# Optimization experiments

Measured on AMD Instinct MI355X. Metric: run time of the kernel, lower is better.

Reference implementation:

```python
import jax, jax.numpy as jnp
import numpy as np

N = 12000       # nodes (Hi-C bins, max_num_nodes)
F_IN = 16       # number_genomic_annotations
HID = 4 * F_IN  # conv1 out = 64
NCLUST = 100    # n_clust
E = 384000      # edges (avg degree 32)


def setup_inputs() -> dict:
    key = jax.random.key(0)
    ks = jax.random.split(key, 8)
    x = jax.random.normal(ks[0], (N, F_IN), dtype=jnp.float32)
    edge_index = jax.random.randint(ks[1], (2, E), 0, N)
    edge_attr = jax.random.uniform(ks[2], (E,), dtype=jnp.float32)
    s1 = 1.0 / np.sqrt(F_IN)
    W1_rel = jax.random.uniform(ks[3], (HID, F_IN), minval=-s1, maxval=s1, dtype=jnp.float32)
    W1_root = jax.random.uniform(ks[4], (HID, F_IN), minval=-s1, maxval=s1, dtype=jnp.float32)
    b1 = jnp.zeros((HID,), jnp.float32)
    s2 = 1.0 / np.sqrt(HID)
    W2_rel = jax.random.uniform(ks[5], (NCLUST, HID), minval=-s2, maxval=s2, dtype=jnp.float32)
    W2_root = jax.random.uniform(ks[6], (NCLUST, HID), minval=-s2, maxval=s2, dtype=jnp.float32)
    b2 = jnp.zeros((NCLUST,), jnp.float32)
    return dict(x=x, edge_index=edge_index, edge_attr=edge_attr,
                W1_rel=W1_rel, W1_root=W1_root, b1=b1,
                W2_rel=W2_rel, W2_root=W2_root, b2=b2)


def _graph_conv(x, src, dst, ew, W_rel, W_root, b):
    # PyG GraphConv (aggr='add'): out = lin_rel(sum_j e_ji * x_j) + lin_root(x)
    msg = x[src] * ew[:, None]                       # [E, F]
    aggr = jax.ops.segment_sum(msg, dst, num_segments=N)  # [N, F]
    return aggr @ W_rel.T + b + x @ W_root.T


def reference(x, edge_index, edge_attr, W1_rel, W1_root, b1, W2_rel, W2_root, b2):
    src, dst = edge_index[0], edge_index[1]
    h = _graph_conv(x, src, dst, edge_attr, W1_rel, W1_root, b1)
    h = jax.nn.relu(h)  # dropout is identity in eval mode
    s_out = _graph_conv(h, src, dst, edge_attr, W2_rel, W2_root, b2)  # [N, NCLUST]

    # to_dense_adj (duplicate edges summed)
    adj = jnp.zeros((N, N), x.dtype).at[src, dst].add(edge_attr)  # [N, N]

    # dense_mincut_pool with S = x (as in the original forward), k = F_IN
    s_mc = jax.nn.softmax(x, axis=-1)      # [N, F_IN]
    as_ = adj @ s_mc                        # [N, F_IN]
    out_adj = s_mc.T @ as_                  # [F_IN, F_IN]
    mincut_num = jnp.trace(out_adj)
    d_flat = adj.sum(-1)                    # [N] degree
    mincut_den = jnp.einsum('ik,i,ik->', s_mc, d_flat, s_mc)  # trace(S^T D S)
    mc = -(mincut_num / mincut_den)

    ss = s_mc.T @ s_mc                      # [F_IN, F_IN]
    i_k = jnp.eye(F_IN, dtype=ss.dtype)
    o = jnp.linalg.norm(ss / jnp.linalg.norm(ss) - i_k / jnp.linalg.norm(i_k))

    return jax.nn.softmax(s_out, axis=-1), mc, o
```

## Files before the change

### kernel.cpp

```cpp
#include <hip/hip_runtime.h>
#include <math.h>

#define N_NODES 12000
#define F_INN 16
#define HIDD 64
#define NCLUST 100
#define NEDGE 384000
#define NBLK_N 47
#define CAP 96
#define EPT 4
#define NTHR_E (NEDGE / EPT)
#define NBLK_E (NTHR_E / 256)
#define NBLK_F1 (N_NODES / 4)

#define OFF_COUNT   0
#define OFF_SCAL    12000
#define ZERO_ELEMS  12002
#define OFF_SSPART  12004
#define OFF_NORM2   24036
#define OFF_W2TREL  36036
#define OFF_W2TROOT 42436
#define OFF_SMC     48836
#define OFF_H       240836
#define OFF_SRCW    1008836

__global__ void zero_kernel(int* __restrict__ ws) {
    int i = blockIdx.x * 256 + threadIdx.x;
    if (i < ZERO_ELEMS) ws[i] = 0;
}

__global__ void phase0_kernel(const float* __restrict__ x, const int* __restrict__ ei,
                              const float* __restrict__ ew, float* __restrict__ smc,
                              float* __restrict__ norm2, int* __restrict__ count,
                              int2* __restrict__ srcw, const float* __restrict__ W2_rel,
                              const float* __restrict__ W2_root, float* __restrict__ w2t_rel,
                              float* __restrict__ w2t_root) {
    __shared__ float fl[6400];
    int t = threadIdx.x;
    int b = blockIdx.x;
    if (b < NBLK_N) {
        int i = b * 256 + t;
        if (i >= N_NODES) return;
        const float4* xr = (const float4*)(x + i * 16);
        float4 r0 = xr[0], r1 = xr[1], r2 = xr[2], r3 = xr[3];
        float v[16] = {r0.x, r0.y, r0.z, r0.w, r1.x, r1.y, r1.z, r1.w,
                       r2.x, r2.y, r2.z, r2.w, r3.x, r3.y, r3.z, r3.w};
        float m = v[0];
#pragma unroll
        for (int k = 1; k < 16; ++k) m = fmaxf(m, v[k]);
        float s = 0.f;
#pragma unroll
        for (int k = 0; k < 16; ++k) { v[k] = __expf(v[k] - m); s += v[k]; }
        float inv = 1.f / s;
        float n2 = 0.f;
#pragma unroll
        for (int k = 0; k < 16; ++k) { v[k] *= inv; n2 += v[k] * v[k]; }
        float4* so = (float4*)(smc + i * 16);
        so[0] = make_float4(v[0], v[1], v[2], v[3]);
        so[1] = make_float4(v[4], v[5], v[6], v[7]);
        so[2] = make_float4(v[8], v[9], v[10], v[11]);
        so[3] = make_float4(v[12], v[13], v[14], v[15]);
        norm2[i] = n2;
    } else if (b < NBLK_N + NBLK_E) {
        int tid = (b - NBLK_N) * 256 + t;
        int e0 = tid * EPT;
        int4 sv = *(const int4*)(ei + e0);
        int4 dv = *(const int4*)(ei + NEDGE + e0);
        float4 wv = *(const float4*)(ew + e0);
        int s[EPT] = {sv.x, sv.y, sv.z, sv.w};
        int d[EPT] = {dv.x, dv.y, dv.z, dv.w};
        float w[EPT] = {wv.x, wv.y, wv.z, wv.w};
        int pos[EPT];
#pragma unroll
        for (int i = 0; i < EPT; ++i) pos[i] = atomicAdd(&count[d[i]], 1);
#pragma unroll
        for (int i = 0; i < EPT; ++i)
            srcw[d[i] * CAP + pos[i]] = make_int2(s[i], __float_as_int(w[i]));
    } else {
        const float* src = (b == NBLK_N + NBLK_E) ? W2_rel : W2_root;
        float* dst = (b == NBLK_N + NBLK_E) ? w2t_rel : w2t_root;
        for (int i = t; i < 6400; i += 256) fl[i] = src[i];
        __syncthreads();
        for (int j = t; j < 6400; j += 256) {
            int kk = j / 100, cl = j - kk * 100;
            dst[j] = fl[cl * 64 + kk];
        }
    }
}

__global__ void fused1_pass2_kernel(const float* __restrict__ x, const int2* __restrict__ srcw,
                                    const int* __restrict__ count, const float* __restrict__ W1_rel,
                                    const float* __restrict__ W1_root, const float* __restrict__ b1,
                                    float* __restrict__ h, const float* __restrict__ smc,
                                    float* __restrict__ sspart, const int* __restrict__ ei,
                                    const float* __restrict__ ew, const float* __restrict__ norm2,
                                    float* __restrict__ scal) {
    __shared__ float shm[4352];
    int t = threadIdx.x;
    int b = blockIdx.x;
    if (b < NBLK_F1) {
        float* wrelT  = shm;
        float* wrootT = shm + 1024;
        float* b1s    = shm + 2048;
        float* aggr   = shm + 2112;
        float* xs     = shm + 2176;
        for (int idx = t; idx < 1024; idx += 256) {
            int f = idx >> 4, k = idx & 15;
            wrelT[(k << 6) + f]  = W1_rel[idx];
            wrootT[(k << 6) + f] = W1_root[idx];
        }
        if (t < 64) b1s[t] = b1[t];
        int w = t >> 6, lane = t & 63;
        int n = b * 4 + w;
        int j = lane >> 4, c = lane & 15;
        int len = count[n];
        const int2* bucket = srcw + n * CAP;
        float acc = 0.f;
        int k = j;
        for (; k + 12 < len; k += 16) {
            int2 p0 = bucket[k], p1 = bucket[k + 4], p2 = bucket[k + 8], p3 = bucket[k + 12];
            float v0 = x[p0.x * 16 + c], v1 = x[p1.x * 16 + c];
            float v2 = x[p2.x * 16 + c], v3 = x[p3.x * 16 + c];
            acc = fmaf(v0, __int_as_float(p0.y), acc);
            acc = fmaf(v1, __int_as_float(p1.y), acc);
            acc = fmaf(v2, __int_as_float(p2.y), acc);
            acc = fmaf(v3, __int_as_float(p3.y), acc);
        }
        for (; k < len; k += 4) {
            int2 p = bucket[k];
            acc = fmaf(x[p.x * 16 + c], __int_as_float(p.y), acc);
        }
        acc += __shfl_down(acc, 32);
        acc += __shfl_down(acc, 16);
        if (lane < 16) { aggr[w * 16 + lane] = acc; xs[w * 16 + lane] = x[n * 16 + lane]; }
        __syncthreads();
        float o = b1s[lane];
#pragma unroll
        for (int kk = 0; kk < 16; ++kk)
            o = fmaf(aggr[w * 16 + kk], wrelT[(kk << 6) + lane],
                     fmaf(xs[w * 16 + kk], wrootT[(kk << 6) + lane], o));
        h[n * 64 + lane] = fmaxf(o, 0.f);
    } else if (b < NBLK_F1 + NBLK_N) {
        int bb = b - NBLK_F1;
        float* rows = shm;
        int n = bb * 256 + t;
        float* rp = rows + t * 17;
        if (n < N_NODES) {
            const float4* sr = (const float4*)(smc + n * 16);
            float4 a0 = sr[0], a1 = sr[1], a2v = sr[2], a3 = sr[3];
            rp[0] = a0.x;  rp[1] = a0.y;  rp[2] = a0.z;  rp[3] = a0.w;
            rp[4] = a1.x;  rp[5] = a1.y;  rp[6] = a1.z;  rp[7] = a1.w;
            rp[8] = a2v.x; rp[9] = a2v.y; rp[10] = a2v.z; rp[11] = a2v.w;
            rp[12] = a3.x; rp[13] = a3.y; rp[14] = a3.z; rp[15] = a3.w;
        } else {
#pragma unroll
            for (int k = 0; k < 16; ++k) rp[k] = 0.f;
        }
        __syncthreads();
        int a = t & 15, bq = t >> 4;
        float accs = 0.f;
#pragma unroll 4
        for (int r = 0; r < 256; ++r)
            accs = fmaf(rows[r * 17 + a], rows[r * 17 + bq], accs);
        sspart[bb * 256 + t] = accs;
    } else {
        int tid = (b - NBLK_F1 - NBLK_N) * 256 + t;
        int e0 = tid * EPT;
        int4 sv = *(const int4*)(ei + e0);
        int4 dv = *(const int4*)(ei + NEDGE + e0);
        float4 wv = *(const float4*)(ew + e0);
        int s[EPT] = {sv.x, sv.y, sv.z, sv.w};
        int d[EPT] = {dv.x, dv.y, dv.z, dv.w};
        float w[EPT] = {wv.x, wv.y, wv.z, wv.w};
        float np = 0.f, dp = 0.f;
#pragma unroll
        for (int i = 0; i < EPT; ++i) {
            const float4* ps = (const float4*)(smc + s[i] * 16);
            const float4* pd = (const float4*)(smc + d[i] * 16);
            float4 s0 = ps[0], s1 = ps[1], s2 = ps[2], s3 = ps[3];
            float4 d0 = pd[0], d1 = pd[1], d2 = pd[2], d3 = pd[3];
            float dot = s0.x * d0.x + s0.y * d0.y + s0.z * d0.z + s0.w * d0.w +
                        s1.x * d1.x + s1.y * d1.y + s1.z * d1.z + s1.w * d1.w +
                        s2.x * d2.x + s2.y * d2.y + s2.z * d2.z + s2.w * d2.w +
                        s3.x * d3.x + s3.y * d3.y + s3.z * d3.z + s3.w * d3.w;
            np = fmaf(w[i], dot, np);
            dp = fmaf(w[i], norm2[s[i]], dp);
        }
        float* redn = shm;
        float* redd = shm + 256;
        redn[t] = np;
        redd[t] = dp;
        __syncthreads();
        for (int s2 = 128; s2 > 0; s2 >>= 1) {
            if (t < s2) { redn[t] += redn[t + s2]; redd[t] += redd[t + s2]; }
            __syncthreads();
        }
        if (t == 0) {
            atomicAdd(&scal[0], redn[0]);
            atomicAdd(&scal[1], redd[0]);
        }
    }
}

__global__ void fused2_finalize_kernel(const float* __restrict__ h, const int2* __restrict__ srcw,
                                       const int* __restrict__ count,
                                       const float* __restrict__ w2t_rel,
                                       const float* __restrict__ w2t_root,
                                       const float* __restrict__ b2, float* __restrict__ out,
                                       const float* __restrict__ sspart,
                                       const float* __restrict__ scal) {
    __shared__ float shm[1328];
    int t = threadIdx.x;
    int b = blockIdx.x;
    if (b < NBLK_F1) {
        float* a2   = shm;
        float* hrow = shm + 256;
        float* logits = shm + 512;
        float* part = shm + 928;
        int nn = t >> 6;
        int c = t & 63;
        int n = b * 4 + nn;
        int len = count[n];
        const int2* bucket = srcw + n * CAP;
        float acc = 0.f;
        int k = 0;
        for (; k + 7 < len; k += 8) {
            int2 p0 = bucket[k],     p1 = bucket[k + 1], p2 = bucket[k + 2], p3 = bucket[k + 3];
            int2 p4 = bucket[k + 4], p5 = bucket[k + 5], p6 = bucket[k + 6], p7 = bucket[k + 7];
            float v0 = h[p0.x * 64 + c], v1 = h[p1.x * 64 + c];
            float v2 = h[p2.x * 64 + c], v3 = h[p3.x * 64 + c];
            float v4 = h[p4.x * 64 + c], v5 = h[p5.x * 64 + c];
            float v6 = h[p6.x * 64 + c], v7 = h[p7.x * 64 + c];
            acc = fmaf(v0, __int_as_float(p0.y), acc);
            acc = fmaf(v1, __int_as_float(p1.y), acc);
            acc = fmaf(v2, __int_as_float(p2.y), acc);
            acc = fmaf(v3, __int_as_float(p3.y), acc);
            acc = fmaf(v4, __int_as_float(p4.y), acc);
            acc = fmaf(v5, __int_as_float(p5.y), acc);
            acc = fmaf(v6, __int_as_float(p6.y), acc);
            acc = fmaf(v7, __int_as_float(p7.y), acc);
        }
        for (; k < len; ++k) {
            int2 p = bucket[k];
            acc = fmaf(h[p.x * 64 + c], __int_as_float(p.y), acc);
        }
        a2[nn * 64 + c] = acc;
        hrow[nn * 64 + c] = h[n * 64 + c];
        __syncthreads();
        int half = t >> 7, c2 = t & 127;
        float p0 = 0.f, p1 = 0.f, p2 = 0.f, p3 = 0.f;
        if (c2 < NCLUST) {
            int kbase = half << 5;
#pragma unroll 8
            for (int kk = kbase; kk < kbase + 32; ++kk) {
                float wr = w2t_rel[kk * 100 + c2];
                float wo = w2t_root[kk * 100 + c2];
                p0 = fmaf(a2[0 * 64 + kk], wr, fmaf(hrow[0 * 64 + kk], wo, p0));
                p1 = fmaf(a2[1 * 64 + kk], wr, fmaf(hrow[1 * 64 + kk], wo, p1));
                p2 = fmaf(a2[2 * 64 + kk], wr, fmaf(hrow[2 * 64 + kk], wo, p2));
                p3 = fmaf(a2[3 * 64 + kk], wr, fmaf(hrow[3 * 64 + kk], wo, p3));
            }
            if (half == 1) {
                part[0 * 100 + c2] = p0;
                part[1 * 100 + c2] = p1;
                part[2 * 100 + c2] = p2;
                part[3 * 100 + c2] = p3;
            }
        }
        __syncthreads();
        if (half == 0 && c2 < NCLUST) {
            float bb = b2[c2];
            logits[0 * 104 + c2] = bb + p0 + part[0 * 100 + c2];
            logits[1 * 104 + c2] = bb + p1 + part[1 * 100 + c2];
            logits[2 * 104 + c2] = bb + p2 + part[2 * 100 + c2];
            logits[3 * 104 + c2] = bb + p3 + part[3 * 100 + c2];
        }
        __syncthreads();
        float v0 = logits[nn * 104 + c];
        float v1 = (c < NCLUST - 64) ? logits[nn * 104 + 64 + c] : -INFINITY;
        float m = fmaxf(v0, v1);
#pragma unroll
        for (int off = 32; off > 0; off >>= 1) m = fmaxf(m, __shfl_xor(m, off));
        float e0 = __expf(v0 - m);
        float e1 = (c < NCLUST - 64) ? __expf(v1 - m) : 0.f;
        float s = e0 + e1;
#pragma unroll
        for (int off = 32; off > 0; off >>= 1) s += __shfl_xor(s, off);
        float inv = 1.f / s;
        out[n * NCLUST + c] = e0 * inv;
        if (c < NCLUST - 64) out[n * NCLUST + 64 + c] = e1 * inv;
    } else {
        float* red = shm;
        float sv = 0.f;
        for (int bb = 0; bb < NBLK_N; ++bb) sv += sspart[bb * 256 + t];
        red[t] = sv * sv;
        __syncthreads();
        for (int s = 128; s > 0; s >>= 1) {
            if (t < s) red[t] += red[t + s];
            __syncthreads();
        }
        float ssnorm = sqrtf(red[0]);
        __syncthreads();
        float diff = sv / ssnorm - ((t % 17 == 0) ? 0.25f : 0.f);
        red[t] = diff * diff;
        __syncthreads();
        for (int s = 128; s > 0; s >>= 1) {
            if (t < s) red[t] += red[t + s];
            __syncthreads();
        }
        if (t == 0) {
            out[N_NODES * NCLUST + 0] = -(scal[0] / scal[1]);
            out[N_NODES * NCLUST + 1] = sqrtf(red[0]);
        }
    }
}

extern "C" void kernel_launch(void* const* d_in, const int* in_sizes, int n_in,
                              void* d_out, int out_size, void* d_ws, size_t ws_size,
                              hipStream_t stream) {
    const float* x       = (const float*)d_in[0];
    const int*   ei      = (const int*)d_in[1];
    const float* ew      = (const float*)d_in[2];
    const float* W1_rel  = (const float*)d_in[3];
    const float* W1_root = (const float*)d_in[4];
    const float* b1      = (const float*)d_in[5];
    const float* W2_rel  = (const float*)d_in[6];
    const float* W2_root = (const float*)d_in[7];
    const float* b2      = (const float*)d_in[8];
    float* out = (float*)d_out;
    int*   wsi = (int*)d_ws;

    int*   count   = wsi + OFF_COUNT;
    float* scal    = (float*)(wsi + OFF_SCAL);
    float* sspart  = (float*)(wsi + OFF_SSPART);
    float* norm2   = (float*)(wsi + OFF_NORM2);
    float* w2trel  = (float*)(wsi + OFF_W2TREL);
    float* w2troot = (float*)(wsi + OFF_W2TROOT);
    float* smc     = (float*)(wsi + OFF_SMC);
    float* h       = (float*)(wsi + OFF_H);
    int2*  srcw    = (int2*)(wsi + OFF_SRCW);

    zero_kernel<<<(ZERO_ELEMS + 255) / 256, 256, 0, stream>>>(wsi);
    phase0_kernel<<<NBLK_N + NBLK_E + 2, 256, 0, stream>>>(x, ei, ew, smc, norm2, count, srcw,
                                                           W2_rel, W2_root, w2trel, w2troot);
    fused1_pass2_kernel<<<NBLK_F1 + NBLK_N + NBLK_E, 256, 0, stream>>>(
        x, srcw, count, W1_rel, W1_root, b1, h, smc, sspart, ei, ew, norm2, scal);
    fused2_finalize_kernel<<<NBLK_F1 + 1, 256, 0, stream>>>(h, srcw, count, w2trel, w2troot, b2,
                                                            out, sspart, scal);
}
```

Baseline: 104.3 us.

## Merge three phase kernels into one persistent kernel with grid barriers

Replaces the three separate phase kernels with a single persistent kernel sized from occupancy (up to 4 blocks per CU times 256), using a software atomic grid barrier between phases. Each phase loops over virtual block indices. Conv1 now broadcasts through wave shuffles instead of shared memory, and the edge loops use different per-thread edge counts. This removes kernel launch gaps and tail effects but adds barrier spin costs and relies on all blocks being co-resident to avoid deadlock.

Result: slower. 282.6 us (+170.9%).

```diff
diff --git a/kernel.cpp b/kernel.cpp
--- a/kernel.cpp
+++ b/kernel.cpp
@@ -6,311 +6,335 @@
 #define HIDD 64
 #define NCLUST 100
 #define NEDGE 384000
-#define NBLK_N 47
 #define CAP 96
-#define EPT 4
-#define NTHR_E (NEDGE / EPT)
-#define NBLK_E (NTHR_E / 256)
-#define NBLK_F1 (N_NODES / 4)
 
 #define OFF_COUNT   0
 #define OFF_SCAL    12000
-#define ZERO_ELEMS  12002
-#define OFF_SSPART  12004
-#define OFF_NORM2   24036
-#define OFF_W2TREL  36036
-#define OFF_W2TROOT 42436
-#define OFF_SMC     48836
-#define OFF_H       240836
-#define OFF_SRCW    1008836
+#define OFF_BAR     12002
+#define ZERO_ELEMS  12008
+#define OFF_SSPART  12008
+#define OFF_NORM2   24040
+#define OFF_W2TREL  36040
+#define OFF_W2TROOT 42440
+#define OFF_SMC     48840
+#define OFF_H       240840
+#define OFF_SRCW    1008840
+
+#define PA_BF   750
+#define PA_SM   (PA_BF + 47)
+#define PA_END  (PA_SM + 2)
+#define PB_F1   3000
+#define PB_SS   (PB_F1 + 47)
+#define PB_END  (PB_SS + 188)
+#define PC_END  3001
 
 __global__ void zero_kernel(int* __restrict__ ws) {
     int i = blockIdx.x * 256 + threadIdx.x;
     if (i < ZERO_ELEMS) ws[i] = 0;
 }
 
-__global__ void phase0_kernel(const float* __restrict__ x, const int* __restrict__ ei,
-                              const float* __restrict__ ew, float* __restrict__ smc,
-                              float* __restrict__ norm2, int* __restrict__ count,
-                              int2* __restrict__ srcw, const float* __restrict__ W2_rel,
-                              const float* __restrict__ W2_root, float* __restrict__ w2t_rel,
-                              float* __restrict__ w2t_root) {
-    __shared__ float fl[6400];
-    int t = threadIdx.x;
-    int b = blockIdx.x;
-    if (b < NBLK_N) {
-        int i = b * 256 + t;
-        if (i >= N_NODES) return;
-        const float4* xr = (const float4*)(x + i * 16);
-        float4 r0 = xr[0], r1 = xr[1], r2 = xr[2], r3 = xr[3];
-        float v[16] = {r0.x, r0.y, r0.z, r0.w, r1.x, r1.y, r1.z, r1.w,
-                       r2.x, r2.y, r2.z, r2.w, r3.x, r3.y, r3.z, r3.w};
-        float m = v[0];
-#pragma unroll
-        for (int k = 1; k < 16; ++k) m = fmaxf(m, v[k]);
-        float s = 0.f;
-#pragma unroll
-        for (int k = 0; k < 16; ++k) { v[k] = __expf(v[k] - m); s += v[k]; }
-        float inv = 1.f / s;
-        float n2 = 0.f;
-#pragma unroll
-        for (int k = 0; k < 16; ++k) { v[k] *= inv; n2 += v[k] * v[k]; }
-        float4* so = (float4*)(smc + i * 16);
-        so[0] = make_float4(v[0], v[1], v[2], v[3]);
-        so[1] = make_float4(v[4], v[5], v[6], v[7]);
-        so[2] = make_float4(v[8], v[9], v[10], v[11]);
-        so[3] = make_float4(v[12], v[13], v[14], v[15]);
-        norm2[i] = n2;
-    } else if (b < NBLK_N + NBLK_E) {
-        int tid = (b - NBLK_N) * 256 + t;
-        int e0 = tid * EPT;
-        int4 sv = *(const int4*)(ei + e0);
-        int4 dv = *(const int4*)(ei + NEDGE + e0);
-        float4 wv = *(const float4*)(ew + e0);
-        int s[EPT] = {sv.x, sv.y, sv.z, sv.w};
-        int d[EPT] = {dv.x, dv.y, dv.z, dv.w};
-        float w[EPT] = {wv.x, wv.y, wv.z, wv.w};
-        int pos[EPT];
-#pragma unroll
-        for (int i = 0; i < EPT; ++i) pos[i] = atomicAdd(&count[d[i]], 1);
-#pragma unroll
-        for (int i = 0; i < EPT; ++i)
-            srcw[d[i] * CAP + pos[i]] = make_int2(s[i], __float_as_int(w[i]));
-    } else {
-        const float* src = (b == NBLK_N + NBLK_E) ? W2_rel : W2_root;
-        float* dst = (b == NBLK_N + NBLK_E) ? w2t_rel : w2t_root;
-        for (int i = t; i < 6400; i += 256) fl[i] = src[i];
-        __syncthreads();
-        for (int j = t; j < 6400; j += 256) {
-            int kk = j / 100, cl = j - kk * 100;
-            dst[j] = fl[cl * 64 + kk];
-        }
-    }
+__device__ inline void grid_barrier(int* cnt, int* gen, int nb) {
+    __syncthreads();
+    if (threadIdx.x == 0) {
+        __threadfence();
+        int g = atomicAdd(gen, 0);
+        if (atomicAdd(cnt, 1) == nb - 1) {
+            atomicExch(cnt, 0);
+            __threadfence();
+            atomicAdd(gen, 1);
+        } else {
+            while (atomicAdd(gen, 0) == g) __builtin_amdgcn_s_sleep(1);
+        }
+        __threadfence();
+    }
+    __syncthreads();
 }
 
-__global__ void fused1_pass2_kernel(const float* __restrict__ x, const int2* __restrict__ srcw,
-                                    const int* __restrict__ count, const float* __restrict__ W1_rel,
-                                    const float* __restrict__ W1_root, const float* __restrict__ b1,
-                                    float* __restrict__ h, const float* __restrict__ smc,
-                                    float* __restrict__ sspart, const int* __restrict__ ei,
-                                    const float* __restrict__ ew, const float* __restrict__ norm2,
-                                    float* __restrict__ scal) {
-    __shared__ float shm[4352];
-    int t = threadIdx.x;
-    int b = blockIdx.x;
-    if (b < NBLK_F1) {
+__global__ __launch_bounds__(256, 4) void mega_kernel(
+    const float* __restrict__ x, const int* __restrict__ ei, const float* __restrict__ ew,
+    const float* __restrict__ W1_rel, const float* __restrict__ W1_root,
+    const float* __restrict__ b1, const float* __restrict__ W2_rel,
+    const float* __restrict__ W2_root, const float* __restrict__ b2,
+    float* __restrict__ out, int* __restrict__ wsi) {
+    __shared__ float shm[6464];
+    const int t = threadIdx.x;
+    const int nb = gridDim.x;
+
+    int*   count    = wsi + OFF_COUNT;
+    float* scal     = (float*)(wsi + OFF_SCAL);
+    int*   bar      = wsi + OFF_BAR;
+    float* sspart   = (float*)(wsi + OFF_SSPART);
+    float* norm2    = (float*)(wsi + OFF_NORM2);
+    float* w2t_rel  = (float*)(wsi + OFF_W2TREL);
+    float* w2t_root = (float*)(wsi + OFF_W2TROOT);
+    float* smc      = (float*)(wsi + OFF_SMC);
+    float* h        = (float*)(wsi + OFF_H);
+    int2*  srcw     = (int2*)(wsi + OFF_SRCW);
+
+    for (int it = blockIdx.x; it < PA_END; it += nb) {
+        if (it < PA_BF) {
+            int tid = it * 256 + t;
+            int e0 = tid * 2;
+            int2 sv = *(const int2*)(ei + e0);
+            int2 dv = *(const int2*)(ei + NEDGE + e0);
+            float2 wv = *(const float2*)(ew + e0);
+            int q0 = atomicAdd(&count[dv.x], 1);
+            srcw[dv.x * CAP + q0] = make_int2(sv.x, __float_as_int(wv.x));
+            int q1 = atomicAdd(&count[dv.y], 1);
+            srcw[dv.y * CAP + q1] = make_int2(sv.y, __float_as_int(wv.y));
+        } else if (it < PA_SM) {
+            int i = (it - PA_BF) * 256 + t;
+            if (i < N_NODES) {
+                const float4* xr = (const float4*)(x + i * 16);
+                float4 r0 = xr[0], r1 = xr[1], r2 = xr[2], r3 = xr[3];
+                float v[16] = {r0.x, r0.y, r0.z, r0.w, r1.x, r1.y, r1.z, r1.w,
+                               r2.x, r2.y, r2.z, r2.w, r3.x, r3.y, r3.z, r3.w};
+                float m = v[0];
+#pragma unroll
+                for (int k = 1; k < 16; ++k) m = fmaxf(m, v[k]);
+                float s = 0.f;
+#pragma unroll
+                for (int k = 0; k < 16; ++k) { v[k] = __expf(v[k] - m); s += v[k]; }
+                float inv = 1.f / s;
+                float n2 = 0.f;
+#pragma unroll
+                for (int k = 0; k < 16; ++k) { v[k] *= inv; n2 += v[k] * v[k]; }
+                float4* so = (float4*)(smc + i * 16);
+                so[0] = make_float4(v[0], v[1], v[2], v[3]);
+                so[1] = make_float4(v[4], v[5], v[6], v[7]);
+                so[2] = make_float4(v[8], v[9], v[10], v[11]);
+                so[3] = make_float4(v[12], v[13], v[14], v[15]);
+                norm2[i] = n2;
+            }
+        } else {
+            const float* srcp = (it == PA_SM) ? W2_rel : W2_root;
+            float* dstp = (it == PA_SM) ? w2t_rel : w2t_root;
+            for (int j2 = t; j2 < 6400; j2 += 256) {
+                int kk = j2 / 100, cl = j2 - kk * 100;
+                dstp[j2] = srcp[cl * 64 + kk];
+            }
+        }
+    }
+    grid_barrier(bar, bar + 1, nb);
+
+    {
         float* wrelT  = shm;
         float* wrootT = shm + 1024;
         float* b1s    = shm + 2048;
-        float* aggr   = shm + 2112;
-        float* xs     = shm + 2176;
         for (int idx = t; idx < 1024; idx += 256) {
             int f = idx >> 4, k = idx & 15;
             wrelT[(k << 6) + f]  = W1_rel[idx];
             wrootT[(k << 6) + f] = W1_root[idx];
         }
         if (t < 64) b1s[t] = b1[t];
-        int w = t >> 6, lane = t & 63;
-        int n = b * 4 + w;
-        int j = lane >> 4, c = lane & 15;
-        int len = count[n];
-        const int2* bucket = srcw + n * CAP;
-        float acc = 0.f;
-        int k = j;
-        for (; k + 12 < len; k += 16) {
-            int2 p0 = bucket[k], p1 = bucket[k + 4], p2 = bucket[k + 8], p3 = bucket[k + 12];
-            float v0 = x[p0.x * 16 + c], v1 = x[p1.x * 16 + c];
-            float v2 = x[p2.x * 16 + c], v3 = x[p3.x * 16 + c];
-            acc = fmaf(v0, __int_as_float(p0.y), acc);
-            acc = fmaf(v1, __int_as_float(p1.y), acc);
-            acc = fmaf(v2, __int_as_float(p2.y), acc);
-            acc = fmaf(v3, __int_as_float(p3.y), acc);
-        }
-        for (; k < len; k += 4) {
-            int2 p = bucket[k];
-            acc = fmaf(x[p.x * 16 + c], __int_as_float(p.y), acc);
-        }
-        acc += __shfl_down(acc, 32);
-        acc += __shfl_down(acc, 16);
-        if (lane < 16) { aggr[w * 16 + lane] = acc; xs[w * 16 + lane] = x[n * 16 + lane]; }
         __syncthreads();
-        float o = b1s[lane];
-#pragma unroll
-        for (int kk = 0; kk < 16; ++kk)
-            o = fmaf(aggr[w * 16 + kk], wrelT[(kk << 6) + lane],
-                     fmaf(xs[w * 16 + kk], wrootT[(kk << 6) + lane], o));
-        h[n * 64 + lane] = fmaxf(o, 0.f);
-    } else if (b < NBLK_F1 + NBLK_N) {
-        int bb = b - NBLK_F1;
-        float* rows = shm;
-        int n = bb * 256 + t;
-        float* rp = rows + t * 17;
-        if (n < N_NODES) {
-            const float4* sr = (const float4*)(smc + n * 16);
-            float4 a0 = sr[0], a1 = sr[1], a2v = sr[2], a3 = sr[3];
-            rp[0] = a0.x;  rp[1] = a0.y;  rp[2] = a0.z;  rp[3] = a0.w;
-            rp[4] = a1.x;  rp[5] = a1.y;  rp[6] = a1.z;  rp[7] = a1.w;
-            rp[8] = a2v.x; rp[9] = a2v.y; rp[10] = a2v.z; rp[11] = a2v.w;
-            rp[12] = a3.x; rp[13] = a3.y; rp[14] = a3.z; rp[15] = a3.w;
-        } else {
-#pragma unroll
-            for (int k = 0; k < 16; ++k) rp[k] = 0.f;
-        }
-        __syncthreads();
-        int a = t & 15, bq = t >> 4;
-        float accs = 0.f;
+        const int w = t >> 6, lane = t & 63;
+        const int j = lane >> 4, c = lane & 15;
+        for (int it = blockIdx.x; it < PB_END; it += nb) {
+            if (it < PB_F1) {
+                int n = it * 4 + w;
+                int len = count[n];
+                const int2* bucket = srcw + n * CAP;
+                float acc = 0.f;
+                int k = j;
+                for (; k + 12 < len; k += 16) {
+                    int2 p0 = bucket[k], p1 = bucket[k + 4], p2 = bucket[k + 8], p3 = bucket[k + 12];
+                    float v0 = x[p0.x * 16 + c], v1 = x[p1.x * 16 + c];
+                    float v2 = x[p2.x * 16 + c], v3 = x[p3.x * 16 + c];
+                    acc = fmaf(v0, __int_as_float(p0.y), acc);
+                    acc = fmaf(v1, __int_as_float(p1.y), acc);
+                    acc = fmaf(v2, __int_as_float(p2.y), acc);
+                    acc = fmaf(v3, __int_as_float(p3.y), acc);
+                }
+                for (; k < len; k += 4) {
+                    int2 p = bucket[k];
+                    acc = fmaf(x[p.x * 16 + c], __int_as_float(p.y), acc);
+                }
+                acc += __shfl_down(acc, 32);
+                acc += __shfl_down(acc, 16);
+                float xval = x[n * 16 + c];
+                float o = b1s[lane];
+#pragma unroll
+                for (int kk = 0; kk < 16; ++kk) {
+                    float ag = __shfl(acc, kk);
+                    float xv = __shfl(xval, kk);
+                    o = fmaf(ag, wrelT[(kk << 6) + lane], fmaf(xv, wrootT[(kk << 6) + lane], o));
+                }
+                h[n * 64 + lane] = fmaxf(o, 0.f);
+            } else if (it < PB_SS) {
+                __syncthreads();
+                float* rows = shm + 2112;
+                int it2 = it - PB_F1;
+                int n = it2 * 256 + t;
+                float* rp = rows + t * 17;
+                if (n < N_NODES) {
+                    const float4* sr = (const float4*)(smc + n * 16);
+                    float4 a0 = sr[0], a1 = sr[1], a2v = sr[2], a3 = sr[3];
+                    rp[0] = a0.x;  rp[1] = a0.y;  rp[2] = a0.z;  rp[3] = a0.w;
+                    rp[4] = a1.x;  rp[5] = a1.y;  rp[6] = a1.z;  rp[7] = a1.w;
+                    rp[8] = a2v.x; rp[9] = a2v.y; rp[10] = a2v.z; rp[11] = a2v.w;
+                    rp[12] = a3.x; rp[13] = a3.y; rp[14] = a3.z; rp[15] = a3.w;
+                } else {
+#pragma unroll
+                    for (int k = 0; k < 16; ++k) rp[k] = 0.f;
+                }
+                __syncthreads();
+                int a = t & 15, bq = t >> 4;
+                float accs = 0.f;
 #pragma unroll 4
-        for (int r = 0; r < 256; ++r)
-            accs = fmaf(rows[r * 17 + a], rows[r * 17 + bq], accs);
-        sspart[bb * 256 + t] = accs;
-    } else {
-        int tid = (b - NBLK_F1 - NBLK_N) * 256 + t;
-        int e0 = tid * EPT;
-        int4 sv = *(const int4*)(ei + e0);
-        int4 dv = *(const int4*)(ei + NEDGE + e0);
-        float4 wv = *(const float4*)(ew + e0);
-        int s[EPT] = {sv.x, sv.y, sv.z, sv.w};
-        int d[EPT] = {dv.x, dv.y, dv.z, dv.w};
-        float w[EPT] = {wv.x, wv.y, wv.z, wv.w};
-        float np = 0.f, dp = 0.f;
-#pragma unroll
-        for (int i = 0; i < EPT; ++i) {
-            const float4* ps = (const float4*)(smc + s[i] * 16);
-            const float4* pd = (const float4*)(smc + d[i] * 16);
-            float4 s0 = ps[0], s1 = ps[1], s2 = ps[2], s3 = ps[3];
-            float4 d0 = pd[0], d1 = pd[1], d2 = pd[2], d3 = pd[3];
-            float dot = s0.x * d0.x + s0.y * d0.y + s0.z * d0.z + s0.w * d0.w +
-                        s1.x * d1.x + s1.y * d1.y + s1.z * d1.z + s1.w * d1.w +
-                        s2.x * d2.x + s2.y * d2.y + s2.z * d2.z + s2.w * d2.w +
-                        s3.x * d3.x + s3.y * d3.y + s3.z * d3.z + s3.w * d3.w;
-            np = fmaf(w[i], dot, np);
-            dp = fmaf(w[i], norm2[s[i]], dp);
-        }
-        float* redn = shm;
-        float* redd = shm + 256;
-        redn[t] = np;
-        redd[t] = dp;
-        __syncthreads();
-        for (int s2 = 128; s2 > 0; s2 >>= 1) {
-            if (t < s2) { redn[t] += redn[t + s2]; redd[t] += redd[t + s2]; }
+                for (int r = 0; r < 256; ++r)
+                    accs = fmaf(rows[r * 17 + a], rows[r * 17 + bq], accs);
+                sspart[it2 * 256 + t] = accs;
+            } else {
+                __syncthreads();
+                int tid = (it - PB_SS) * 256 + t;
+                int e0 = tid * 8;
+                float np = 0.f, dp = 0.f;
+                if (e0 < NEDGE) {
+                    int4 sa = *(const int4*)(ei + e0);
+                    int4 sb = *(const int4*)(ei + e0 + 4);
+                    int4 da = *(const int4*)(ei + NEDGE + e0);
+                    int4 db = *(const int4*)(ei + NEDGE + e0 + 4);
+                    float4 wa = *(const float4*)(ew + e0);
+                    float4 wb = *(const float4*)(ew + e0 + 4);
+                    int s8[8] = {sa.x, sa.y, sa.z, sa.w, sb.x, sb.y, sb.z, sb.w};
+                    int d8[8] = {da.x, da.y, da.z, da.w, db.x, db.y, db.z, db.w};
+                    float w8[8] = {wa.x, wa.y, wa.z, wa.w, wb.x, wb.y, wb.z, wb.w};
+#pragma unroll
+                    for (int u = 0; u < 8; ++u) {
+                        const float4* ps = (const float4*)(smc + s8[u] * 16);
+                        const float4* pd = (const float4*)(smc + d8[u] * 16);
+                        float4 s0 = ps[0], s1 = ps[1], s2 = ps[2], s3 = ps[3];
+                        float4 d0 = pd[0], d1 = pd[1], d2 = pd[2], d3 = pd[3];
+                        float dot = s0.x * d0.x + s0.y * d0.y + s0.z * d0.z + s0.w * d0.w +
+                                    s1.x * d1.x + s1.y * d1.y + s1.z * d1.z + s1.w * d1.w +
+                                    s2.x * d2.x + s2.y * d2.y + s2.z * d2.z + s2.w * d2.w +
+                                    s3.x * d3.x + s3.y * d3.y + s3.z * d3.z + s3.w * d3.w;
+                        np = fmaf(w8[u], dot, np);
+                        dp = fmaf(w8[u], norm2[s8[u]], dp);
+                    }
+                }
+                float* redn = shm + 2112;
+                float* redd = shm + 2368;
+                redn[t] = np;
+                redd[t] = dp;
+                __syncthreads();
+                for (int s2 = 128; s2 > 0; s2 >>= 1) {
+                    if (t < s2) { redn[t] += redn[t + s2]; redd[t] += redd[t + s2]; }
+                    __syncthreads();
+                }
+                if (t == 0) {
+                    atomicAdd(&scal[0], redn[0]);
+                    atomicAdd(&scal[1], redd[0]);
+                }
+            }
+        }
+    }
+    grid_barrier(bar, bar + 1, nb);
+
+    {
+        const int nn = t >> 6, c = t & 63;
+        const int half = t >> 7, c2 = t & 127;
+        for (int it = blockIdx.x; it < PC_END; it += nb) {
             __syncthreads();
-        }
-        if (t == 0) {
-            atomicAdd(&scal[0], redn[0]);
-            atomicAdd(&scal[1], redd[0]);
-        }
-    }
-}
-
-__global__ void fused2_finalize_kernel(const float* __restrict__ h, const int2* __restrict__ srcw,
-                                       const int* __restrict__ count,
-                                       const float* __restrict__ w2t_rel,
-                                       const float* __restrict__ w2t_root,
-                                       const float* __restrict__ b2, float* __restrict__ out,
-                                       const float* __restrict__ sspart,
-                                       const float* __restrict__ scal) {
-    __shared__ float shm[1328];
-    int t = threadIdx.x;
-    int b = blockIdx.x;
-    if (b < NBLK_F1) {
-        float* a2   = shm;
-        float* hrow = shm + 256;
-        float* logits = shm + 512;
-        float* part = shm + 928;
-        int nn = t >> 6;
-        int c = t & 63;
-        int n = b * 4 + nn;
-        int len = count[n];
-        const int2* bucket = srcw + n * CAP;
-        float acc = 0.f;
-        int k = 0;
-        for (; k + 7 < len; k += 8) {
-            int2 p0 = bucket[k],     p1 = bucket[k + 1], p2 = bucket[k + 2], p3 = bucket[k + 3];
-            int2 p4 = bucket[k + 4], p5 = bucket[k + 5], p6 = bucket[k + 6], p7 = bucket[k + 7];
-            float v0 = h[p0.x * 64 + c], v1 = h[p1.x * 64 + c];
-            float v2 = h[p2.x * 64 + c], v3 = h[p3.x * 64 + c];
-            float v4 = h[p4.x * 64 + c], v5 = h[p5.x * 64 + c];
-            float v6 = h[p6.x * 64 + c], v7 = h[p7.x * 64 + c];
-            acc = fmaf(v0, __int_as_float(p0.y), acc);
-            acc = fmaf(v1, __int_as_float(p1.y), acc);
-            acc = fmaf(v2, __int_as_float(p2.y), acc);
-            acc = fmaf(v3, __int_as_float(p3.y), acc);
-            acc = fmaf(v4, __int_as_float(p4.y), acc);
-            acc = fmaf(v5, __int_as_float(p5.y), acc);
-            acc = fmaf(v6, __int_as_float(p6.y), acc);
-            acc = fmaf(v7, __int_as_float(p7.y), acc);
-        }
-        for (; k < len; ++k) {
-            int2 p = bucket[k];
-            acc = fmaf(h[p.x * 64 + c], __int_as_float(p.y), acc);
-        }
-        a2[nn * 64 + c] = acc;
-        hrow[nn * 64 + c] = h[n * 64 + c];
-        __syncthreads();
-        int half = t >> 7, c2 = t & 127;
-        float p0 = 0.f, p1 = 0.f, p2 = 0.f, p3 = 0.f;
-        if (c2 < NCLUST) {
-            int kbase = half << 5;
+            if (it < PB_F1) {
+                float* a2     = shm;
+                float* hrow   = shm + 256;
+                float* logits = shm + 512;
+                float* part   = shm + 928;
+                int n = it * 4 + nn;
+                int len = count[n];
+                const int2* bucket = srcw + n * CAP;
+                float acc = 0.f;
+                int k = 0;
+                for (; k + 7 < len; k += 8) {
+                    int2 p0 = bucket[k],     p1 = bucket[k + 1], p2 = bucket[k + 2], p3 = bucket[k + 3];
+                    int2 p4 = bucket[k + 4], p5 = bucket[k + 5], p6 = bucket[k + 6], p7 = bucket[k + 7];
+                    float v0 = h[p0.x * 64 + c], v1 = h[p1.x * 64 + c];
+                    float v2 = h[p2.x * 64 + c], v3 = h[p3.x * 64 + c];
+                    float v4 = h[p4.x * 64 + c], v5 = h[p5.x * 64 + c];
+                    float v6 = h[p6.x * 64 + c], v7 = h[p7.x * 64 + c];
+                    acc = fmaf(v0, __int_as_float(p0.y), acc);
+                    acc = fmaf(v1, __int_as_float(p1.y), acc);
+                    acc = fmaf(v2, __int_as_float(p2.y), acc);
+                    acc = fmaf(v3, __int_as_float(p3.y), acc);
+                    acc = fmaf(v4, __int_as_float(p4.y), acc);
+                    acc = fmaf(v5, __int_as_float(p5.y), acc);
+                    acc = fmaf(v6, __int_as_float(p6.y), acc);
+                    acc = fmaf(v7, __int_as_float(p7.y), acc);
+                }
+                for (; k < len; ++k) {
+                    int2 p = bucket[k];
+                    acc = fmaf(h[p.x * 64 + c], __int_as_float(p.y), acc);
+                }
+                a2[nn * 64 + c] = acc;
+                hrow[nn * 64 + c] = h[n * 64 + c];
+                __syncthreads();
+                float p0 = 0.f, p1 = 0.f, p2 = 0.f, p3 = 0.f;
+                if (c2 < NCLUST) {
+                    int kbase = half << 5;
 #pragma unroll 8
-            for (int kk = kbase; kk < kbase + 32; ++kk) {
-                float wr = w2t_rel[kk * 100 + c2];
-                float wo = w2t_root[kk * 100 + c2];
-                p0 = fmaf(a2[0 * 64 + kk], wr, fmaf(hrow[0 * 64 + kk], wo, p0));
-                p1 = fmaf(a2[1 * 64 + kk], wr, fmaf(hrow[1 * 64 + kk], wo, p1));
-                p2 = fmaf(a2[2 * 64 + kk], wr, fmaf(hrow[2 * 64 + kk], wo, p2));
-                p3 = fmaf(a2[3 * 64 + kk], wr, fmaf(hrow[3 * 64 + kk], wo, p3));
+                    for (int kk = kbase; kk < kbase + 32; ++kk) {
+                        float wr = w2t_rel[kk * 100 + c2];
+                        float wo = w2t_root[kk * 100 + c2];
+                        p0 = fmaf(a2[0 * 64 + kk], wr, fmaf(hrow[0 * 64 + kk], wo, p0));
+                        p1 = fmaf(a2[1 * 64 + kk], wr, fmaf(hrow[1 * 64 + kk], wo, p1));
+                        p2 = fmaf(a2[2 * 64 + kk], wr, fmaf(hrow[2 * 64 + kk], wo, p2));
+                        p3 = fmaf(a2[3 * 64 + kk], wr, fmaf(hrow[3 * 64 + kk], wo, p3));
+                    }
+                    if (half == 1) {
+                        part[0 * 100 + c2] = p0;
+                        part[1 * 100 + c2] = p1;
+                        part[2 * 100 + c2] = p2;
+                        part[3 * 100 + c2] = p3;
+                    }
+                }
+                __syncthreads();
+                if (half == 0 && c2 < NCLUST) {
+                    float bb2 = b2[c2];
+                    logits[0 * 104 + c2] = bb2 + p0 + part[0 * 100 + c2];
+                    logits[1 * 104 + c2] = bb2 + p1 + part[1 * 100 + c2];
+                    logits[2 * 104 + c2] = bb2 + p2 + part[2 * 100 + c2];
+                    logits[3 * 104 + c2] = bb2 + p3 + part[3 * 100 + c2];
+                }
+                __syncthreads();
+                float v0 = logits[nn * 104 + c];
+                float v1 = (c < NCLUST - 64) ? logits[nn * 104 + 64 + c] : -INFINITY;
+                float m = fmaxf(v0, v1);
+#pragma unroll
+                for (int off = 32; off > 0; off >>= 1) m = fmaxf(m, __shfl_xor(m, off));
+                float e0 = __expf(v0 - m);
+                float e1 = (c < NCLUST - 64) ? __expf(v1 - m) : 0.f;
+                float s = e0 + e1;
+#pragma unroll
+                for (int off = 32; off > 0; off >>= 1) s += __shfl_xor(s, off);
+                float inv = 1.f / s;
+                out[n * NCLUST + c] = e0 * inv;
+                if (c < NCLUST - 64) out[n * NCLUST + 64 + c] = e1 * inv;
+            } else {
+                float* red = shm;
+                float sv = 0.f;
+                for (int bb = 0; bb < 47; ++bb) sv += sspart[bb * 256 + t];
+                red[t] = sv * sv;
+                __syncthreads();
+                for (int s = 128; s > 0; s >>= 1) {
+                    if (t < s) red[t] += red[t + s];
+                    __syncthreads();
+                }
+                float ssnorm = sqrtf(red[0]);
+                __syncthreads();
+                float diff = sv / ssnorm - ((t % 17 == 0) ? 0.25f : 0.f);
+                red[t] = diff * diff;
+                __syncthreads();
+                for (int s = 128; s > 0; s >>= 1) {
+                    if (t < s) red[t] += red[t + s];
+                    __syncthreads();
+                }
+                if (t == 0) {
+                    out[N_NODES * NCLUST + 0] = -(scal[0] / scal[1]);
+                    out[N_NODES * NCLUST + 1] = sqrtf(red[0]);
+                }
             }
-            if (half == 1) {
-                part[0 * 100 + c2] = p0;
-                part[1 * 100 + c2] = p1;
-                part[2 * 100 + c2] = p2;
-                part[3 * 100 + c2] = p3;
-            }
-        }
-        __syncthreads();
-        if (half == 0 && c2 < NCLUST) {
-            float bb = b2[c2];
-            logits[0 * 104 + c2] = bb + p0 + part[0 * 100 + c2];
-            logits[1 * 104 + c2] = bb + p1 + part[1 * 100 + c2];
-            logits[2 * 104 + c2] = bb + p2 + part[2 * 100 + c2];
-            logits[3 * 104 + c2] = bb + p3 + part[3 * 100 + c2];
-        }
-        __syncthreads();
-        float v0 = logits[nn * 104 + c];
-        float v1 = (c < NCLUST - 64) ? logits[nn * 104 + 64 + c] : -INFINITY;
-        float m = fmaxf(v0, v1);
-#pragma unroll
-        for (int off = 32; off > 0; off >>= 1) m = fmaxf(m, __shfl_xor(m, off));
-        float e0 = __expf(v0 - m);
-        float e1 = (c < NCLUST - 64) ? __expf(v1 - m) : 0.f;
-        float s = e0 + e1;
-#pragma unroll
-        for (int off = 32; off > 0; off >>= 1) s += __shfl_xor(s, off);
-        float inv = 1.f / s;
-        out[n * NCLUST + c] = e0 * inv;
-        if (c < NCLUST - 64) out[n * NCLUST + 64 + c] = e1 * inv;
-    } else {
-        float* red = shm;
-        float sv = 0.f;
-        for (int bb = 0; bb < NBLK_N; ++bb) sv += sspart[bb * 256 + t];
-        red[t] = sv * sv;
-        __syncthreads();
-        for (int s = 128; s > 0; s >>= 1) {
-            if (t < s) red[t] += red[t + s];
-            __syncthreads();
-        }
-        float ssnorm = sqrtf(red[0]);
-        __syncthreads();
-        float diff = sv / ssnorm - ((t % 17 == 0) ? 0.25f : 0.f);
-        red[t] = diff * diff;
-        __syncthreads();
-        for (int s = 128; s > 0; s >>= 1) {
-            if (t < s) red[t] += red[t + s];
-            __syncthreads();
-        }
-        if (t == 0) {
-            out[N_NODES * NCLUST + 0] = -(scal[0] / scal[1]);
-            out[N_NODES * NCLUST + 1] = sqrtf(red[0]);
         }
     }
 }
@@ -330,21 +354,17 @@
     float* out = (float*)d_out;
     int*   wsi = (int*)d_ws;
 
-    int*   count   = wsi + OFF_COUNT;
-    float* scal    = (float*)(wsi + OFF_SCAL);
-    float* sspart  = (float*)(wsi + OFF_SSPART);
-    float* norm2   = (float*)(wsi + OFF_NORM2);
-    float* w2trel  = (float*)(wsi + OFF_W2TREL);
-    float* w2troot = (float*)(wsi + OFF_W2TROOT);
-    float* smc     = (float*)(wsi + OFF_SMC);
-    float* h       = (float*)(wsi + OFF_H);
-    int2*  srcw    = (int2*)(wsi + OFF_SRCW);
+    static int g_grid = 0;
+    if (g_grid == 0) {
+        int maxb = 0;
+        hipError_t e = hipOccupancyMaxActiveBlocksPerMultiprocessor(
+            &maxb, (const void*)mega_kernel, 256, 0);
+        if (e != hipSuccess || maxb < 1) maxb = 1;
+        if (maxb > 4) maxb = 4;
+        g_grid = maxb * 256;
+    }
 
     zero_kernel<<<(ZERO_ELEMS + 255) / 256, 256, 0, stream>>>(wsi);
-    phase0_kernel<<<NBLK_N + NBLK_E + 2, 256, 0, stream>>>(x, ei, ew, smc, norm2, count, srcw,
-                                                           W2_rel, W2_root, w2trel, w2troot);
-    fused1_pass2_kernel<<<NBLK_F1 + NBLK_N + NBLK_E, 256, 0, stream>>>(
-        x, srcw, count, W1_rel, W1_root, b1, h, smc, sspart, ei, ew, norm2, scal);
-    fused2_finalize_kernel<<<NBLK_F1 + 1, 256, 0, stream>>>(h, srcw, count, w2trel, w2troot, b2,
-                                                            out, sspart, scal);
+    mega_kernel<<<g_grid, 256, 0, stream>>>(x, ei, ew, W1_rel, W1_root, b1,
+                                            W2_rel, W2_root, b2, out, wsi);
 }
```
